# Kernel optimization log

Hardware: AMD Instinct MI355X
Metric: run time of the kernel (lower is better)

Reference implementation:

```python
import jax, jax.numpy as jnp
from jax import lax
import numpy as np

B, H, W, D_MODEL = 2, 64, 64, 192
D_INNER, D_STATE, DT_RANK = 384, 16, 12
L = H * W
LN_EPS = 1e-5


def setup_inputs() -> dict:
    ks = jax.random.split(jax.random.key(0), 12)
    rng = np.random.default_rng(0)
    perm = rng.permutation(L).astype(np.int32)

    def p(i, shape, scale=0.02):
        return jax.random.normal(ks[i], shape, dtype=jnp.float32) * scale

    return {
        "x": jax.random.normal(ks[0], (B, H, W, D_MODEL), dtype=jnp.float32),
        "condition": jax.random.normal(ks[1], (B, H, W, D_MODEL), dtype=jnp.float32),
        "W_in": p(2, (2 * D_INNER, D_MODEL)),
        "W_con": p(3, (D_INNER, D_MODEL)),
        "conv_w": p(4, (D_INNER, 1, 3, 3)),
        "conv_b": jnp.zeros((D_INNER,), jnp.float32),
        "con_conv_w": p(5, (D_INNER, 1, 3, 3)),
        "con_conv_b": jnp.zeros((D_INNER,), jnp.float32),
        "x_proj_w": p(6, (DT_RANK + 2 * D_STATE, D_INNER)),
        "dt_proj_w": p(7, (D_INNER, DT_RANK)),
        "dt_proj_b": p(8, (D_INNER,), 0.1),
        "A_logs": jnp.tile(jnp.log(jnp.arange(1, D_STATE + 1, dtype=jnp.float32))[None, :], (D_INNER, 1)),
        "Ds": jnp.ones((D_INNER,), jnp.float32),
        "ln_w": jnp.ones((D_INNER,), jnp.float32),
        "ln_b": jnp.zeros((D_INNER,), jnp.float32),
        "W_out": p(9, (D_MODEL, D_INNER)),
        "scan_path": jnp.asarray(perm),
        "rev_scan_path": jnp.asarray(np.argsort(perm).astype(np.int32)),
    }


def _dwconv(x, w, b):
    # depthwise 3x3 conv, SAME padding; x: [B, C, H, W], w: [C, 1, 3, 3]
    y = lax.conv_general_dilated(x, w, (1, 1), "SAME",
                                 dimension_numbers=("NCHW", "OIHW", "NCHW"),
                                 feature_group_count=x.shape[1])
    return y + b[None, :, None, None]


def _selective_scan(u, delta, A, Bs, Cs, D):
    # u, delta: [B, D, L]; A: [D, N]; Bs, Cs: [B, N, L]; D: [D]
    dA = jnp.exp(jnp.einsum("bdl,dn->lbdn", delta, A))          # [L, B, D, N]
    dBu = jnp.einsum("bdl,bnl,bdl->lbdn", delta, Bs, u)          # [L, B, D, N]
    Ct = jnp.transpose(Cs, (2, 0, 1))                             # [L, B, N]
    h0 = jnp.zeros(dA.shape[1:], dA.dtype)

    def step(h, inp):
        a, b, c = inp
        h = a * h + b
        return h, jnp.einsum("bdn,bn->bd", h, c)

    _, ys = lax.scan(step, h0, (dA, dBu, Ct))                     # ys: [L, B, D]
    y = jnp.transpose(ys, (1, 2, 0))                              # [B, D, L]
    return y + u * D[None, :, None]


def _forward(x, condition, W_in, W_con, conv_w, conv_b, con_conv_w, con_conv_b,
             x_proj_w, dt_proj_w, dt_proj_b, A_logs, Ds, ln_w, ln_b, W_out,
             scan_path, rev_scan_path):
    b, h, w, _ = x.shape
    l = h * w
    xz = x @ W_in.T                                               # [B, H, W, 2*Din]
    xa, z = jnp.split(xz, 2, axis=-1)
    z = jax.nn.silu(z)
    c = condition @ W_con.T
    xa = jax.nn.silu(_dwconv(jnp.transpose(xa, (0, 3, 1, 2)), conv_w, conv_b))
    c = jax.nn.silu(_dwconv(jnp.transpose(c, (0, 3, 1, 2)), con_conv_w, con_conv_b))
    d = xa.shape[1]
    xs = xa.reshape(b, d, l)[:, :, scan_path]                     # forward_permutation, K=1
    cs = c.reshape(b, d, l)[:, :, scan_path]
    x_dbl = jnp.einsum("bdl,cd->bcl", xs + cs, x_proj_w)          # [B, R+2N, L]
    r, n = dt_proj_w.shape[1], A_logs.shape[1]
    dts = jnp.einsum("brl,dr->bdl", x_dbl[:, :r], dt_proj_w)
    Bs = x_dbl[:, r:r + n]
    Cs = x_dbl[:, r + n:]
    A = -jnp.exp(A_logs)
    delta = jax.nn.softplus(dts + dt_proj_b[None, :, None])       # delta_softplus=True
    y = _selective_scan(xs, delta, A, Bs, Cs, Ds)                 # [B, D, L]
    y = y[:, :, rev_scan_path]                                    # backward_permutation
    y = jnp.transpose(y, (0, 2, 1))                               # [B, L, D]
    mu = jnp.mean(y, axis=-1, keepdims=True)
    var = jnp.var(y, axis=-1, keepdims=True)
    y = (y - mu) * lax.rsqrt(var + LN_EPS) * ln_w + ln_b          # out_norm
    y = y.reshape(b, h, w, d) * z
    return y @ W_out.T                                            # out_proj (no bias)


def reference(x, condition, W_in, W_con, conv_w, conv_b, con_conv_w, con_conv_b,
              x_proj_w, dt_proj_w, dt_proj_b, A_logs, Ds, ln_w, ln_b, W_out,
              scan_path, rev_scan_path):
    return _forward(x, condition, W_in, W_con, conv_w, conv_b, con_conv_w,
                    con_conv_b, x_proj_w, dt_proj_w, dt_proj_b, A_logs, Ds,
                    ln_w, ln_b, W_out, scan_path, rev_scan_path)
```

## Files before the change

kernel.cpp:

```cpp
#include <hip/hip_runtime.h>
#include <math.h>

#define BB 2
#define HH 64
#define WW 64
#define DM 192
#define DI 384
#define NS 16
#define DTR 12
#define LL 4096
#define ROWS (BB*LL)
#define NCHUNK 128
#define LCHUNK 32
#define NCOMB 448
#define CSTRIDE ((size_t)BB * DI * 8)

typedef __attribute__((ext_vector_type(8))) short bf16x8;
typedef __attribute__((ext_vector_type(4))) float f32x4;

typedef __attribute__((address_space(3))) void        as3_void;
typedef __attribute__((address_space(1))) const void  as1_cvoid;

__device__ __forceinline__ void gl_lds16(const unsigned short* g, unsigned short* l) {
    __builtin_amdgcn_global_load_lds((as1_cvoid*)g, (as3_void*)l, 16, 0, 0);
}

__device__ __forceinline__ float silu_f(float v) {
    return v / (1.0f + __expf(-v));
}

__device__ __forceinline__ unsigned short f2bf(float f) {
    union { float f; unsigned int u; } c; c.f = f;
    unsigned int u = c.u;
    u += 0x7fffu + ((u >> 16) & 1u);
    return (unsigned short)(u >> 16);
}
__device__ __forceinline__ float bf2f(unsigned short h) {
    union { unsigned int u; float f; } c; c.u = ((unsigned int)h) << 16;
    return c.f;
}

__global__ __launch_bounds__(256) void prep_weights(
    const float* __restrict__ x, const float* __restrict__ cond,
    const float* __restrict__ w_in, const float* __restrict__ w_con,
    const float* __restrict__ w_out,
    const float* __restrict__ x_proj_w, const float* __restrict__ dt_w,
    unsigned short* __restrict__ w_in_bf, unsigned short* __restrict__ w_con_bf,
    unsigned short* __restrict__ w_out_bf, unsigned short* __restrict__ wc,
    unsigned short* __restrict__ x_bfo, unsigned short* __restrict__ c_bfo)
{
    int idx = blockIdx.x * 256 + threadIdx.x;
    if (idx < 73728) {
        const float4* src; ushort4* dst; int off;
        if (idx < 36864)      { src = (const float4*)w_in;  dst = (ushort4*)w_in_bf;  off = idx; }
        else if (idx < 55296) { src = (const float4*)w_con; dst = (ushort4*)w_con_bf; off = idx - 36864; }
        else                  { src = (const float4*)w_out; dst = (ushort4*)w_out_bf; off = idx - 55296; }
        float4 v = src[off];
        ushort4 o;
        o.x = f2bf(v.x); o.y = f2bf(v.y); o.z = f2bf(v.z); o.w = f2bf(v.w);
        dst[off] = o;
    } else if (idx < 73728 + NCOMB * DI) {
        int e = idx - 73728;
        int row = e / DI, k = e - row * DI;
        float v = 0.f;
        if (row < 384) {
            const float* dw = dt_w + row * DTR;
            #pragma unroll
            for (int r = 0; r < DTR; ++r) v += dw[r] * x_proj_w[r * DI + k];
        } else if (row < 416) {
            v = x_proj_w[(12 + (row - 384)) * DI + k];
        }
        wc[e] = f2bf(v);
    } else if (idx < 73728 + NCOMB * DI + 786432) {
        int e = idx - (73728 + NCOMB * DI);
        const float4* src; ushort4* dst; int off;
        if (e < 393216) { src = (const float4*)x;    dst = (ushort4*)x_bfo; off = e; }
        else            { src = (const float4*)cond; dst = (ushort4*)c_bfo; off = e - 393216; }
        float4 v = src[off];
        ushort4 o;
        o.x = f2bf(v.x); o.y = f2bf(v.y); o.z = f2bf(v.z); o.w = f2bf(v.w);
        dst[off] = o;
    }
}

__global__ __launch_bounds__(256) void gemm_in(
    const unsigned short* __restrict__ x_bf, const unsigned short* __restrict__ cin_bf,
    const unsigned short* __restrict__ w_in_bf,
    const unsigned short* __restrict__ w_con_bf,
    unsigned short* __restrict__ xa_bf, unsigned short* __restrict__ z_bf,
    unsigned short* __restrict__ c_bf)
{
    const int zz = blockIdx.z;
    if (zz == 1 && blockIdx.y >= 6) return;
    const unsigned short* A = zz ? cin_bf : x_bf;
    const unsigned short* W = zz ? w_con_bf : w_in_bf;

    __shared__ __align__(16) unsigned short sA[128 * 32];
    __shared__ __align__(16) unsigned short sB[64 * 32];
    const int bm = blockIdx.x * 128;
    const int bn = blockIdx.y * 64;
    const int tid  = threadIdx.x;
    const int wave = tid >> 6;
    const int lane = tid & 63;
    const int quad = lane >> 4;
    const int l16  = lane & 15;
    const int srow = tid >> 2;
    const int scol = (tid & 3) * 8;

    f32x4 acc[2][4];
    #pragma unroll
    for (int rf = 0; rf < 2; ++rf)
        #pragma unroll
        for (int t = 0; t < 4; ++t) acc[rf][t] = (f32x4)(0.f);

    const unsigned short* gA0 = &A[(size_t)(bm + srow) * DM + scol];
    const unsigned short* gA1 = gA0 + (size_t)64 * DM;
    const unsigned short* gB  = &W[(size_t)(bn + srow) * DM + scol];
    unsigned short* lA0 = &sA[wave * 512];
    unsigned short* lA1 = &sA[2048 + wave * 512];
    unsigned short* lB  = &sB[wave * 512];

    const int ar0 = (wave * 32 + l16) * 32 + quad * 8;
    const int ar1 = ar0 + 16 * 32;

    for (int k0 = 0; k0 < DM; k0 += 32) {
        gl_lds16(gA0 + k0, lA0);
        gl_lds16(gA1 + k0, lA1);
        gl_lds16(gB  + k0, lB);
        __syncthreads();
        bf16x8 a0 = *(bf16x8*)&sA[ar0];
        bf16x8 a1 = *(bf16x8*)&sA[ar1];
        #pragma unroll
        for (int t = 0; t < 4; ++t) {
            bf16x8 b = *(bf16x8*)&sB[(t * 16 + l16) * 32 + quad * 8];
            acc[0][t] = __builtin_amdgcn_mfma_f32_16x16x32_bf16(a0, b, acc[0][t], 0, 0, 0);
            acc[1][t] = __builtin_amdgcn_mfma_f32_16x16x32_bf16(a1, b, acc[1][t], 0, 0, 0);
        }
        __syncthreads();
    }

    #pragma unroll
    for (int rf = 0; rf < 2; ++rf) {
        #pragma unroll
        for (int t = 0; t < 4; ++t) {
            int col = bn + t * 16 + l16;
            #pragma unroll
            for (int r = 0; r < 4; ++r) {
                int row = bm + wave * 32 + rf * 16 + quad * 4 + r;
                float v = acc[rf][t][r];
                if (zz == 0) {
                    if (col < 384) xa_bf[(size_t)row * 384 + col] = f2bf(v);
                    else           z_bf[(size_t)row * 384 + (col - 384)] = f2bf(silu_f(v));
                } else {
                    c_bf[(size_t)row * 384 + col] = f2bf(v);
                }
            }
        }
    }
}

__global__ __launch_bounds__(256) void gemm_comb(
    const unsigned short* __restrict__ A, const unsigned short* __restrict__ W,
    const float* __restrict__ bias, float* __restrict__ btct,
    unsigned short* __restrict__ du_lo)
{
    __shared__ __align__(16) unsigned short sA[128 * 32];
    __shared__ __align__(16) unsigned short sB[64 * 32];
    const int bm = blockIdx.x * 128;
    const int bn = blockIdx.y * 64;
    const int tid  = threadIdx.x;
    const int wave = tid >> 6;
    const int lane = tid & 63;
    const int quad = lane >> 4;
    const int l16  = lane & 15;
    const int srow = tid >> 2;
    const int scol = (tid & 3) * 8;

    f32x4 acc[2][4];
    #pragma unroll
    for (int rf = 0; rf < 2; ++rf)
        #pragma unroll
        for (int t = 0; t < 4; ++t) acc[rf][t] = (f32x4)(0.f);

    const unsigned short* gA0 = &A[(size_t)(bm + srow) * DI + scol];
    const unsigned short* gA1 = gA0 + (size_t)64 * DI;
    const unsigned short* gB  = &W[(size_t)(bn + srow) * DI + scol];
    unsigned short* lA0 = &sA[wave * 512];
    unsigned short* lA1 = &sA[2048 + wave * 512];
    unsigned short* lB  = &sB[wave * 512];

    const int ar0 = (wave * 32 + l16) * 32 + quad * 8;
    const int ar1 = ar0 + 16 * 32;

    for (int k0 = 0; k0 < DI; k0 += 32) {
        gl_lds16(gA0 + k0, lA0);
        gl_lds16(gA1 + k0, lA1);
        gl_lds16(gB  + k0, lB);
        __syncthreads();
        bf16x8 a0 = *(bf16x8*)&sA[ar0];
        bf16x8 a1 = *(bf16x8*)&sA[ar1];
        #pragma unroll
        for (int t = 0; t < 4; ++t) {
            bf16x8 b = *(bf16x8*)&sB[(t * 16 + l16) * 32 + quad * 8];
            acc[0][t] = __builtin_amdgcn_mfma_f32_16x16x32_bf16(a0, b, acc[0][t], 0, 0, 0);
            acc[1][t] = __builtin_amdgcn_mfma_f32_16x16x32_bf16(a1, b, acc[1][t], 0, 0, 0);
        }
        __syncthreads();
    }

    #pragma unroll
    for (int rf = 0; rf < 2; ++rf) {
        #pragma unroll
        for (int t = 0; t < 4; ++t) {
            int col = bn + t * 16 + l16;
            #pragma unroll
            for (int r = 0; r < 4; ++r) {
                int row = bm + wave * 32 + rf * 16 + quad * 4 + r;
                float v = acc[rf][t][r];
                if (col < 384) {
                    float a = v + bias[col];
                    float sp = (a > 20.f) ? a : log1pf(__expf(a));
                    du_lo[((size_t)row * 384 + col) * 2] = f2bf(sp);
                } else if (col < 416) {
                    int idx = col - 384;
                    int pos = (idx < 16) ? ((idx & 7) * 4 + (idx >> 3))
                                         : (((idx - 16) & 7) * 4 + 2 + ((idx - 16) >> 3));
                    btct[(size_t)row * 32 + pos] = v;
                }
            }
        }
    }
}

__global__ __launch_bounds__(256) void gemm_outk(
    const unsigned short* __restrict__ A, const unsigned short* __restrict__ W,
    float* __restrict__ out)
{
    __shared__ __align__(16) unsigned short sA[64 * 32];
    __shared__ __align__(16) unsigned short sB[64 * 32];
    const int bm = blockIdx.x * 64;
    const int bn = blockIdx.y * 64;
    const int tid  = threadIdx.x;
    const int wave = tid >> 6;
    const int lane = tid & 63;
    const int quad = lane >> 4;
    const int l16  = lane & 15;
    const int srow = tid >> 2;
    const int scol = (tid & 3) * 8;

    f32x4 acc[4];
    #pragma unroll
    for (int t = 0; t < 4; ++t) acc[t] = (f32x4)(0.f);

    const unsigned short* gA = &A[(size_t)(bm + srow) * DI + scol];
    const unsigned short* gB = &W[(size_t)(bn + srow) * DI + scol];
    unsigned short* lA = &sA[wave * 512];
    unsigned short* lB = &sB[wave * 512];

    const int arow = (wave * 16 + l16) * 32 + quad * 8;

    for (int k0 = 0; k0 < DI; k0 += 32) {
        gl_lds16(gA + k0, lA);
        gl_lds16(gB + k0, lB);
        __syncthreads();
        bf16x8 a = *(bf16x8*)&sA[arow];
        #pragma unroll
        for (int t = 0; t < 4; ++t) {
            bf16x8 b = *(bf16x8*)&sB[(t * 16 + l16) * 32 + quad * 8];
            acc[t] = __builtin_amdgcn_mfma_f32_16x16x32_bf16(a, b, acc[t], 0, 0, 0);
        }
        __syncthreads();
    }

    #pragma unroll
    for (int t = 0; t < 4; ++t) {
        int col = bn + t * 16 + l16;
        #pragma unroll
        for (int r = 0; r < 4; ++r) {
            int row = bm + wave * 16 + quad * 4 + r;
            out[(size_t)row * DM + col] = acc[t][r];
        }
    }
}

__global__ __launch_bounds__(256) void dwconv2_scatter(
    const unsigned short* __restrict__ xin, const unsigned short* __restrict__ cin,
    const float* __restrict__ wx, const float* __restrict__ bx,
    const float* __restrict__ wc, const float* __restrict__ bc,
    const int* __restrict__ rev_scan_path,
    unsigned short* __restrict__ du_hi,
    unsigned short* __restrict__ s_bf)
{
    const int tile = blockIdx.x;
    const int c0   = blockIdx.y * 32;
    const int b    = blockIdx.z;
    const int h0 = (tile >> 3) * 8, w0 = (tile & 7) * 8;
    __shared__ float smx[10 * 10 * 32];
    __shared__ float smc[10 * 10 * 32];
    __shared__ int   jtile[64];

    for (int idx = threadIdx.x; idx < 3200; idx += 256) {
        int pix = idx >> 5, ch = idx & 31;
        int py = pix / 10, px = pix - py * 10;
        int gh = h0 + py - 1, gw = w0 + px - 1;
        float vx = 0.f, vc = 0.f;
        if (gh >= 0 && gh < 64 && gw >= 0 && gw < 64) {
            size_t g = ((size_t)(b * LL + gh * 64 + gw)) * DI + c0 + ch;
            vx = bf2f(xin[g]); vc = bf2f(cin[g]);
        }
        smx[idx] = vx; smc[idx] = vc;
    }
    if (threadIdx.x < 64) {
        int l = (h0 + (threadIdx.x >> 3)) * 64 + (w0 + (threadIdx.x & 7));
        jtile[threadIdx.x] = rev_scan_path[l];
    }
    __syncthreads();

    const int ch = threadIdx.x & 31;
    const int pq = threadIdx.x >> 5;
    float wrx[9], wrc[9];
    #pragma unroll
    for (int k = 0; k < 9; ++k) {
        wrx[k] = wx[(c0 + ch) * 9 + k];
        wrc[k] = wc[(c0 + ch) * 9 + k];
    }
    const float bvx = bx[c0 + ch];
    const float bvc = bc[c0 + ch];

    #pragma unroll
    for (int i = 0; i < 8; ++i) {
        int p  = pq * 8 + i;
        int ph = p >> 3, pw = p & 7;
        float ax = bvx, ac = bvc;
        #pragma unroll
        for (int ki = 0; ki < 3; ++ki)
            #pragma unroll
            for (int kj = 0; kj < 3; ++kj) {
                int si = ((ph + ki) * 10 + (pw + kj)) * 32 + ch;
                ax += wrx[ki * 3 + kj] * smx[si];
                ac += wrc[ki * 3 + kj] * smc[si];
            }
        float xv = silu_f(ax);
        float sv = xv + silu_f(ac);
        size_t o = ((size_t)(b * LL + jtile[p])) * DI + c0 + ch;
        du_hi[o * 2 + 1] = f2bf(xv);
        s_bf[o]          = f2bf(sv);
    }
}

__global__ __launch_bounds__(256) void scan_chunkA(
    const unsigned int* __restrict__ du, const float* __restrict__ btct,
    const float* __restrict__ A_logs,
    float* __restrict__ chunkA, float* __restrict__ chunkB)
{
    const int c = blockIdx.x;
    const int g = blockIdx.y;
    const int b = blockIdx.z;
    const int t = threadIdx.x;
    const int grp = t >> 3, p = t & 7;
    const int d = g * 32 + grp;
    const float Av0 = -__expf(A_logs[d * NS + p]);
    const float Av1 = -__expf(A_logs[d * NS + p + 8]);
    const int j0 = c * LCHUNK;

    const unsigned int* dul = du + ((size_t)b * LL + j0) * DI + d;
    const float2*       bl  = (const float2*)btct + ((size_t)b * LL + j0) * 16 + p * 2;

    float h0 = 0.f, h1 = 0.f, Sd = 0.f;
    unsigned int duv[4]; float2 bv[4];
    #pragma unroll
    for (int q = 0; q < 4; ++q) {
        duv[q] = dul[(size_t)q * DI]; bv[q] = bl[(size_t)q * 16];
    }
    for (int j = 0; j < LCHUNK; j += 4) {
        unsigned int ndu[4]; float2 nb[4];
        if (j + 4 < LCHUNK) {
            #pragma unroll
            for (int q = 0; q < 4; ++q) {
                int jj = j + 4 + q;
                ndu[q] = dul[(size_t)jj * DI]; nb[q] = bl[(size_t)jj * 16];
            }
        }
        #pragma unroll
        for (int q = 0; q < 4; ++q) {
            float dv = bf2f((unsigned short)(duv[q] & 0xffff));
            float uv = bf2f((unsigned short)(duv[q] >> 16));
            float e0 = __expf(dv * Av0);
            float e1 = __expf(dv * Av1);
            float duu = dv * uv;
            h0 = e0 * h0 + bv[q].x * duu;
            h1 = e1 * h1 + bv[q].y * duu;
            Sd += dv;
        }
        #pragma unroll
        for (int q = 0; q < 4; ++q) { duv[q]=ndu[q]; bv[q]=nb[q]; }
    }
    size_t idx = (size_t)c * CSTRIDE + ((size_t)b * DI + d) * 8 + p;
    ((float2*)chunkA)[idx] = make_float2(__expf(Sd * Av0), __expf(Sd * Av1));
    ((float2*)chunkB)[idx] = make_float2(h0, h1);
}

__global__ __launch_bounds__(256) void scan_chunkC(
    const unsigned int* __restrict__ du, const float* __restrict__ btct,
    const float* __restrict__ A_logs, const float* __restrict__ Ds,
    const float* __restrict__ chunkA, const float* __restrict__ chunkB,
    unsigned short* __restrict__ yt)
{
    const int c = blockIdx.x;
    const int g = blockIdx.y;
    const int b = blockIdx.z;
    const int t = threadIdx.x;
    const int grp = t >> 3, p = t & 7;
    const int d = g * 32 + grp;
    const float Av0 = -__expf(A_logs[d * NS + p]);
    const float Av1 = -__expf(A_logs[d * NS + p + 8]);
    const float Dv = Ds[d];
    const int j0 = c * LCHUNK;

    const unsigned int* dul = du + ((size_t)b * LL + j0) * DI + d;
    const float4*       bcl = (const float4*)btct + ((size_t)b * LL + j0) * 8 + p;
    unsigned short* yl = yt + ((size_t)b * LL + j0) * DI + d;

    const size_t off = ((size_t)b * DI + d) * 8 + p;
    const float2* A2 = (const float2*)chunkA;
    const float2* B2 = (const float2*)chunkB;
    float h0 = 0.f, h1 = 0.f, P0 = 1.f, P1 = 1.f;
    for (int i = c - 1; i >= 0; --i) {
        size_t ix = (size_t)i * CSTRIDE + off;
        float2 a = A2[ix], bv = B2[ix];
        h0 += P0 * bv.x;  h1 += P1 * bv.y;
        P0 *= a.x;        P1 *= a.y;
        if (fmaxf(fabsf(P0), fabsf(P1)) < 1e-30f) break;
    }

    unsigned int duv[4]; float4 bc[4];
    #pragma unroll
    for (int q = 0; q < 4; ++q) {
        duv[q] = dul[(size_t)q * DI]; bc[q] = bcl[(size_t)q * 8];
    }
    for (int j = 0; j < LCHUNK; j += 4) {
        unsigned int ndu[4]; float4 nbc[4];
        if (j + 4 < LCHUNK) {
            #pragma unroll
            for (int q = 0; q < 4; ++q) {
                int jj = j + 4 + q;
                ndu[q] = dul[(size_t)jj * DI]; nbc[q] = bcl[(size_t)jj * 8];
            }
        }
        #pragma unroll
        for (int q = 0; q < 4; ++q) {
            float dv = bf2f((unsigned short)(duv[q] & 0xffff));
            float uv = bf2f((unsigned short)(duv[q] >> 16));
            float e0 = __expf(dv * Av0);
            float e1 = __expf(dv * Av1);
            float duu = dv * uv;
            h0 = e0 * h0 + bc[q].x * duu;
            h1 = e1 * h1 + bc[q].y * duu;
            float acc = h0 * bc[q].z + h1 * bc[q].w;
            acc += __shfl_xor(acc, 4, 8);
            acc += __shfl_xor(acc, 2, 8);
            acc += __shfl_xor(acc, 1, 8);
            if (p == 0) yl[(size_t)(j + q) * DI] = f2bf(acc + uv * Dv);
        }
        #pragma unroll
        for (int q = 0; q < 4; ++q) { duv[q]=ndu[q]; bc[q]=nbc[q]; }
    }
}

__global__ __launch_bounds__(128) void ln_mul(
    const unsigned short* __restrict__ yt, const unsigned short* __restrict__ z,
    const int* __restrict__ scan_path,
    const float* __restrict__ ln_w, const float* __restrict__ ln_b,
    unsigned short* __restrict__ yn)
{
    const int j = blockIdx.x;
    const int b = blockIdx.y;
    const int l = scan_path[j];
    const int t = threadIdx.x;
    const unsigned short* row = yt + ((size_t)(b * LL + j)) * DI;
    float v0 = bf2f(row[t]), v1 = bf2f(row[t + 128]), v2 = bf2f(row[t + 256]);
    float s  = v0 + v1 + v2;
    float s2 = v0*v0 + v1*v1 + v2*v2;
    #pragma unroll
    for (int off = 32; off > 0; off >>= 1) {
        s  += __shfl_down(s, off);
        s2 += __shfl_down(s2, off);
    }
    __shared__ float red[4];
    if ((t & 63) == 0) { red[(t >> 6) * 2] = s; red[(t >> 6) * 2 + 1] = s2; }
    __syncthreads();
    float S  = red[0] + red[2];
    float S2 = red[1] + red[3];
    float mu  = S * (1.0f / DI);
    float var = S2 * (1.0f / DI) - mu * mu;
    float inv = rsqrtf(var + 1e-5f);

    const unsigned short* zr = z + ((size_t)(b * LL + l)) * DI;
    unsigned short* o = yn + ((size_t)(b * LL + l)) * DI;
    o[t]       = f2bf(((v0 - mu) * inv * ln_w[t]       + ln_b[t])       * bf2f(zr[t]));
    o[t + 128] = f2bf(((v1 - mu) * inv * ln_w[t + 128] + ln_b[t + 128]) * bf2f(zr[t + 128]));
    o[t + 256] = f2bf(((v2 - mu) * inv * ln_w[t + 256] + ln_b[t + 256]) * bf2f(zr[t + 256]));
}

extern "C" void kernel_launch(void* const* d_in, const int* in_sizes, int n_in,
                              void* d_out, int out_size, void* d_ws, size_t ws_size,
                              hipStream_t stream) {
    const float* x          = (const float*)d_in[0];
    const float* cond       = (const float*)d_in[1];
    const float* W_in       = (const float*)d_in[2];
    const float* W_con      = (const float*)d_in[3];
    const float* conv_w     = (const float*)d_in[4];
    const float* conv_b     = (const float*)d_in[5];
    const float* con_conv_w = (const float*)d_in[6];
    const float* con_conv_b = (const float*)d_in[7];
    const float* x_proj_w   = (const float*)d_in[8];
    const float* dt_proj_w  = (const float*)d_in[9];
    const float* dt_proj_b  = (const float*)d_in[10];
    const float* A_logs     = (const float*)d_in[11];
    const float* Ds         = (const float*)d_in[12];
    const float* ln_w       = (const float*)d_in[13];
    const float* ln_b       = (const float*)d_in[14];
    const float* W_out      = (const float*)d_in[15];
    const int*   scan_path  = (const int*)d_in[16];
    const int*   rev_path   = (const int*)d_in[17];

    float* ws = (float*)d_ws;
    const size_t S  = (size_t)BB * LL * DI;
    const size_t SC = (size_t)NCHUNK * BB * DI * NS;
    float* ytslab  = ws + 0 * S;
    float* zslab   = ws + 1 * S;
    float* ynslab  = ws + 2 * S;
    float* duslab  = ws + 3 * S;
    float* btct    = ws + 4 * S;
    float* chunkA  = btct + (size_t)BB * LL * 32;
    float* chunkB  = chunkA + SC;
    float* bfpool  = chunkB + SC;

    unsigned short* yt_bf    = (unsigned short*)ytslab;
    unsigned short* z_bf     = (unsigned short*)zslab;
    unsigned short* yn_bf    = (unsigned short*)ynslab;
    unsigned int*   du       = (unsigned int*)duslab;
    unsigned short* s_bf     = (unsigned short*)bfpool;
    unsigned short* xa_bf    = s_bf + (size_t)ROWS * DI;
    unsigned short* c_bf     = xa_bf + (size_t)ROWS * DI;
    unsigned short* w_in_bf  = c_bf + (size_t)ROWS * DI;
    unsigned short* w_con_bf = w_in_bf + 768 * DM;
    unsigned short* w_out_bf = w_con_bf + 384 * DM;
    unsigned short* wcomb_bf = w_out_bf + 192 * DI;
    unsigned short* x_bf2    = wcomb_bf + (size_t)NCOMB * DI;
    unsigned short* cin_bf2  = x_bf2 + (size_t)ROWS * DM;

    prep_weights<<<4032, 256, 0, stream>>>(
        x, cond, W_in, W_con, W_out, x_proj_w, dt_proj_w,
        w_in_bf, w_con_bf, w_out_bf, wcomb_bf, x_bf2, cin_bf2);

    gemm_in<<<dim3(ROWS / 128, 12, 2), 256, 0, stream>>>(
        x_bf2, cin_bf2, w_in_bf, w_con_bf, xa_bf, z_bf, c_bf);
    dwconv2_scatter<<<dim3(64, 12, BB), 256, 0, stream>>>(
        xa_bf, c_bf, conv_w, conv_b, con_conv_w, con_conv_b,
        rev_path, (unsigned short*)du, s_bf);
    gemm_comb<<<dim3(ROWS / 128, NCOMB / 64), 256, 0, stream>>>(
        s_bf, wcomb_bf, dt_proj_b, btct, (unsigned short*)du);
    scan_chunkA<<<dim3(NCHUNK, DI / 32, BB), 256, 0, stream>>>(
        du, btct, A_logs, chunkA, chunkB);
    scan_chunkC<<<dim3(NCHUNK, DI / 32, BB), 256, 0, stream>>>(
        du, btct, A_logs, Ds, chunkA, chunkB, yt_bf);
    ln_mul<<<dim3(LL, BB), 128, 0, stream>>>(yt_bf, z_bf, scan_path, ln_w, ln_b, yn_bf);
    gemm_outk<<<dim3(ROWS / 64, DM / 64), 256, 0, stream>>>(yn_bf, w_out_bf, (float*)d_out);
}
```

Before: 206.6 us.

## Fuse LayerNorm and gating into out-projection GEMM, widen input GEMM tiles

```diff
diff --git a/kernel.cpp b/kernel.cpp
--- a/kernel.cpp
+++ b/kernel.cpp
@@ -12,7 +12,7 @@
 #define ROWS (BB*LL)
 #define NCHUNK 128
 #define LCHUNK 32
-#define NCOMB 448
+#define NCOMBP 512
 #define CSTRIDE ((size_t)BB * DI * 8)
 
 typedef __attribute__((ext_vector_type(8))) short bf16x8;
@@ -59,7 +59,7 @@
         ushort4 o;
         o.x = f2bf(v.x); o.y = f2bf(v.y); o.z = f2bf(v.z); o.w = f2bf(v.w);
         dst[off] = o;
-    } else if (idx < 73728 + NCOMB * DI) {
+    } else if (idx < 73728 + NCOMBP * DI) {
         int e = idx - 73728;
         int row = e / DI, k = e - row * DI;
         float v = 0.f;
@@ -71,8 +71,8 @@
             v = x_proj_w[(12 + (row - 384)) * DI + k];
         }
         wc[e] = f2bf(v);
-    } else if (idx < 73728 + NCOMB * DI + 786432) {
-        int e = idx - (73728 + NCOMB * DI);
+    } else if (idx < 73728 + NCOMBP * DI + 786432) {
+        int e = idx - (73728 + NCOMBP * DI);
         const float4* src; ushort4* dst; int off;
         if (e < 393216) { src = (const float4*)x;    dst = (ushort4*)x_bfo; off = e; }
         else            { src = (const float4*)cond; dst = (ushort4*)c_bfo; off = e - 393216; }
@@ -91,14 +91,14 @@
     unsigned short* __restrict__ c_bf)
 {
     const int zz = blockIdx.z;
-    if (zz == 1 && blockIdx.y >= 6) return;
+    if (zz == 1 && blockIdx.y >= 3) return;
     const unsigned short* A = zz ? cin_bf : x_bf;
     const unsigned short* W = zz ? w_con_bf : w_in_bf;
 
     __shared__ __align__(16) unsigned short sA[128 * 32];
-    __shared__ __align__(16) unsigned short sB[64 * 32];
+    __shared__ __align__(16) unsigned short sB[128 * 32];
     const int bm = blockIdx.x * 128;
-    const int bn = blockIdx.y * 64;
+    const int bn = blockIdx.y * 128;
     const int tid  = threadIdx.x;
     const int wave = tid >> 6;
     const int lane = tid & 63;
@@ -107,18 +107,20 @@
     const int srow = tid >> 2;
     const int scol = (tid & 3) * 8;
 
-    f32x4 acc[2][4];
+    f32x4 acc[2][8];
     #pragma unroll
     for (int rf = 0; rf < 2; ++rf)
         #pragma unroll
-        for (int t = 0; t < 4; ++t) acc[rf][t] = (f32x4)(0.f);
+        for (int t = 0; t < 8; ++t) acc[rf][t] = (f32x4)(0.f);
 
     const unsigned short* gA0 = &A[(size_t)(bm + srow) * DM + scol];
     const unsigned short* gA1 = gA0 + (size_t)64 * DM;
-    const unsigned short* gB  = &W[(size_t)(bn + srow) * DM + scol];
+    const unsigned short* gB0 = &W[(size_t)(bn + srow) * DM + scol];
+    const unsigned short* gB1 = gB0 + (size_t)64 * DM;
     unsigned short* lA0 = &sA[wave * 512];
     unsigned short* lA1 = &sA[2048 + wave * 512];
-    unsigned short* lB  = &sB[wave * 512];
+    unsigned short* lB0 = &sB[wave * 512];
+    unsigned short* lB1 = &sB[2048 + wave * 512];
 
     const int ar0 = (wave * 32 + l16) * 32 + quad * 8;
     const int ar1 = ar0 + 16 * 32;
@@ -126,12 +128,13 @@
     for (int k0 = 0; k0 < DM; k0 += 32) {
         gl_lds16(gA0 + k0, lA0);
         gl_lds16(gA1 + k0, lA1);
-        gl_lds16(gB  + k0, lB);
+        gl_lds16(gB0 + k0, lB0);
+        gl_lds16(gB1 + k0, lB1);
         __syncthreads();
         bf16x8 a0 = *(bf16x8*)&sA[ar0];
         bf16x8 a1 = *(bf16x8*)&sA[ar1];
         #pragma unroll
-        for (int t = 0; t < 4; ++t) {
+        for (int t = 0; t < 8; ++t) {
             bf16x8 b = *(bf16x8*)&sB[(t * 16 + l16) * 32 + quad * 8];
             acc[0][t] = __builtin_amdgcn_mfma_f32_16x16x32_bf16(a0, b, acc[0][t], 0, 0, 0);
             acc[1][t] = __builtin_amdgcn_mfma_f32_16x16x32_bf16(a1, b, acc[1][t], 0, 0, 0);
@@ -142,7 +145,7 @@
     #pragma unroll
     for (int rf = 0; rf < 2; ++rf) {
         #pragma unroll
-        for (int t = 0; t < 4; ++t) {
+        for (int t = 0; t < 8; ++t) {
             int col = bn + t * 16 + l16;
             #pragma unroll
             for (int r = 0; r < 4; ++r) {
@@ -165,9 +168,9 @@
     unsigned short* __restrict__ du_lo)
 {
     __shared__ __align__(16) unsigned short sA[128 * 32];
-    __shared__ __align__(16) unsigned short sB[64 * 32];
+    __shared__ __align__(16) unsigned short sB[128 * 32];
     const int bm = blockIdx.x * 128;
-    const int bn = blockIdx.y * 64;
+    const int bn = blockIdx.y * 128;
     const int tid  = threadIdx.x;
     const int wave = tid >> 6;
     const int lane = tid & 63;
@@ -176,18 +179,20 @@
     const int srow = tid >> 2;
     const int scol = (tid & 3) * 8;
 
-    f32x4 acc[2][4];
+    f32x4 acc[2][8];
     #pragma unroll
     for (int rf = 0; rf < 2; ++rf)
         #pragma unroll
-        for (int t = 0; t < 4; ++t) acc[rf][t] = (f32x4)(0.f);
+        for (int t = 0; t < 8; ++t) acc[rf][t] = (f32x4)(0.f);
 
     const unsigned short* gA0 = &A[(size_t)(bm + srow) * DI + scol];
     const unsigned short* gA1 = gA0 + (size_t)64 * DI;
-    const unsigned short* gB  = &W[(size_t)(bn + srow) * DI + scol];
+    const unsigned short* gB0 = &W[(size_t)(bn + srow) * DI + scol];
+    const unsigned short* gB1 = gB0 + (size_t)64 * DI;
     unsigned short* lA0 = &sA[wave * 512];
     unsigned short* lA1 = &sA[2048 + wave * 512];
-    unsigned short* lB  = &sB[wave * 512];
+    unsigned short* lB0 = &sB[wave * 512];
+    unsigned short* lB1 = &sB[2048 + wave * 512];
 
     const int ar0 = (wave * 32 + l16) * 32 + quad * 8;
     const int ar1 = ar0 + 16 * 32;
@@ -195,12 +200,13 @@
     for (int k0 = 0; k0 < DI; k0 += 32) {
         gl_lds16(gA0 + k0, lA0);
         gl_lds16(gA1 + k0, lA1);
-        gl_lds16(gB  + k0, lB);
+        gl_lds16(gB0 + k0, lB0);
+        gl_lds16(gB1 + k0, lB1);
         __syncthreads();
         bf16x8 a0 = *(bf16x8*)&sA[ar0];
         bf16x8 a1 = *(bf16x8*)&sA[ar1];
         #pragma unroll
-        for (int t = 0; t < 4; ++t) {
+        for (int t = 0; t < 8; ++t) {
             bf16x8 b = *(bf16x8*)&sB[(t * 16 + l16) * 32 + quad * 8];
             acc[0][t] = __builtin_amdgcn_mfma_f32_16x16x32_bf16(a0, b, acc[0][t], 0, 0, 0);
             acc[1][t] = __builtin_amdgcn_mfma_f32_16x16x32_bf16(a1, b, acc[1][t], 0, 0, 0);
@@ -211,7 +217,7 @@
     #pragma unroll
     for (int rf = 0; rf < 2; ++rf) {
         #pragma unroll
-        for (int t = 0; t < 4; ++t) {
+        for (int t = 0; t < 8; ++t) {
             int col = bn + t * 16 + l16;
             #pragma unroll
             for (int r = 0; r < 4; ++r) {
@@ -232,42 +238,83 @@
     }
 }
 
-__global__ __launch_bounds__(256) void gemm_outk(
-    const unsigned short* __restrict__ A, const unsigned short* __restrict__ W,
-    float* __restrict__ out)
-{
-    __shared__ __align__(16) unsigned short sA[64 * 32];
+__global__ __launch_bounds__(256) void gemm_out_fused(
+    const unsigned short* __restrict__ yt, const unsigned short* __restrict__ z,
+    const int* __restrict__ rev_path,
+    const float* __restrict__ ln_w, const float* __restrict__ ln_b,
+    const unsigned short* __restrict__ W, float* __restrict__ out)
+{
+    __shared__ __align__(16) unsigned short sA[64 * 392];
     __shared__ __align__(16) unsigned short sB[64 * 32];
     const int bm = blockIdx.x * 64;
     const int bn = blockIdx.y * 64;
-    const int tid  = threadIdx.x;
+    const int tid = threadIdx.x;
+    const int r   = tid >> 2;
+    const int q4  = tid & 3;
+    const int b   = bm >> 12;
+    const int l   = (bm & (LL - 1)) + r;
+    const int js  = rev_path[l];
+
+    const unsigned short* yrow = yt + ((size_t)(b * LL + js)) * DI;
+    const unsigned short* zrow = z  + ((size_t)(b * LL + l)) * DI;
+
+    float s = 0.f, s2 = 0.f;
+    #pragma unroll
+    for (int i = 0; i < 12; ++i) {
+        bf16x8 v = *(const bf16x8*)&yrow[i * 32 + q4 * 8];
+        #pragma unroll
+        for (int e = 0; e < 8; ++e) {
+            float f = bf2f((unsigned short)v[e]);
+            s += f; s2 += f * f;
+        }
+    }
+    s  += __shfl_xor(s, 1);  s  += __shfl_xor(s, 2);
+    s2 += __shfl_xor(s2, 1); s2 += __shfl_xor(s2, 2);
+    const float mu  = s * (1.0f / DI);
+    const float inv = rsqrtf(s2 * (1.0f / DI) - mu * mu + 1e-5f);
+
+    #pragma unroll
+    for (int i = 0; i < 12; ++i) {
+        int c = i * 32 + q4 * 8;
+        bf16x8 v  = *(const bf16x8*)&yrow[c];
+        bf16x8 zv = *(const bf16x8*)&zrow[c];
+        float4 wa = *(const float4*)&ln_w[c];
+        float4 wb = *(const float4*)&ln_w[c + 4];
+        float4 ba = *(const float4*)&ln_b[c];
+        float4 bb = *(const float4*)&ln_b[c + 4];
+        bf16x8 o;
+        o[0] = (short)f2bf(((bf2f((unsigned short)v[0]) - mu) * inv * wa.x + ba.x) * bf2f((unsigned short)zv[0]));
+        o[1] = (short)f2bf(((bf2f((unsigned short)v[1]) - mu) * inv * wa.y + ba.y) * bf2f((unsigned short)zv[1]));
+        o[2] = (short)f2bf(((bf2f((unsigned short)v[2]) - mu) * inv * wa.z + ba.z) * bf2f((unsigned short)zv[2]));
+        o[3] = (short)f2bf(((bf2f((unsigned short)v[3]) - mu) * inv * wa.w + ba.w) * bf2f((unsigned short)zv[3]));
+        o[4] = (short)f2bf(((bf2f((unsigned short)v[4]) - mu) * inv * wb.x + bb.x) * bf2f((unsigned short)zv[4]));
+        o[5] = (short)f2bf(((bf2f((unsigned short)v[5]) - mu) * inv * wb.y + bb.y) * bf2f((unsigned short)zv[5]));
+        o[6] = (short)f2bf(((bf2f((unsigned short)v[6]) - mu) * inv * wb.z + bb.z) * bf2f((unsigned short)zv[6]));
+        o[7] = (short)f2bf(((bf2f((unsigned short)v[7]) - mu) * inv * wb.w + bb.w) * bf2f((unsigned short)zv[7]));
+        *(bf16x8*)&sA[r * 392 + c] = o;
+    }
+
     const int wave = tid >> 6;
     const int lane = tid & 63;
     const int quad = lane >> 4;
     const int l16  = lane & 15;
-    const int srow = tid >> 2;
-    const int scol = (tid & 3) * 8;
 
     f32x4 acc[4];
     #pragma unroll
     for (int t = 0; t < 4; ++t) acc[t] = (f32x4)(0.f);
 
-    const unsigned short* gA = &A[(size_t)(bm + srow) * DI + scol];
-    const unsigned short* gB = &W[(size_t)(bn + srow) * DI + scol];
-    unsigned short* lA = &sA[wave * 512];
+    const unsigned short* gB = &W[(size_t)(bn + r) * DI + q4 * 8];
     unsigned short* lB = &sB[wave * 512];
-
-    const int arow = (wave * 16 + l16) * 32 + quad * 8;
+    const int abase = (wave * 16 + l16) * 392 + quad * 8;
 
     for (int k0 = 0; k0 < DI; k0 += 32) {
-        gl_lds16(gA + k0, lA);
         gl_lds16(gB + k0, lB);
         __syncthreads();
-        bf16x8 a = *(bf16x8*)&sA[arow];
+        bf16x8 a = *(bf16x8*)&sA[abase + k0];
         #pragma unroll
         for (int t = 0; t < 4; ++t) {
-            bf16x8 b = *(bf16x8*)&sB[(t * 16 + l16) * 32 + quad * 8];
-            acc[t] = __builtin_amdgcn_mfma_f32_16x16x32_bf16(a, b, acc[t], 0, 0, 0);
+            bf16x8 bfr = *(bf16x8*)&sB[(t * 16 + l16) * 32 + quad * 8];
+            acc[t] = __builtin_amdgcn_mfma_f32_16x16x32_bf16(a, bfr, acc[t], 0, 0, 0);
         }
         __syncthreads();
     }
@@ -276,9 +323,9 @@
     for (int t = 0; t < 4; ++t) {
         int col = bn + t * 16 + l16;
         #pragma unroll
-        for (int r = 0; r < 4; ++r) {
-            int row = bm + wave * 16 + quad * 4 + r;
-            out[(size_t)row * DM + col] = acc[t][r];
+        for (int rr = 0; rr < 4; ++rr) {
+            int row = bm + wave * 16 + quad * 4 + rr;
+            out[(size_t)row * DM + col] = acc[t][rr];
         }
     }
 }
@@ -465,41 +512,6 @@
         #pragma unroll
         for (int q = 0; q < 4; ++q) { duv[q]=ndu[q]; bc[q]=nbc[q]; }
     }
-}
-
-__global__ __launch_bounds__(128) void ln_mul(
-    const unsigned short* __restrict__ yt, const unsigned short* __restrict__ z,
-    const int* __restrict__ scan_path,
-    const float* __restrict__ ln_w, const float* __restrict__ ln_b,
-    unsigned short* __restrict__ yn)
-{
-    const int j = blockIdx.x;
-    const int b = blockIdx.y;
-    const int l = scan_path[j];
-    const int t = threadIdx.x;
-    const unsigned short* row = yt + ((size_t)(b * LL + j)) * DI;
-    float v0 = bf2f(row[t]), v1 = bf2f(row[t + 128]), v2 = bf2f(row[t + 256]);
-    float s  = v0 + v1 + v2;
-    float s2 = v0*v0 + v1*v1 + v2*v2;
-    #pragma unroll
-    for (int off = 32; off > 0; off >>= 1) {
-        s  += __shfl_down(s, off);
-        s2 += __shfl_down(s2, off);
-    }
-    __shared__ float red[4];
-    if ((t & 63) == 0) { red[(t >> 6) * 2] = s; red[(t >> 6) * 2 + 1] = s2; }
-    __syncthreads();
-    float S  = red[0] + red[2];
-    float S2 = red[1] + red[3];
-    float mu  = S * (1.0f / DI);
-    float var = S2 * (1.0f / DI) - mu * mu;
-    float inv = rsqrtf(var + 1e-5f);
-
-    const unsigned short* zr = z + ((size_t)(b * LL + l)) * DI;
-    unsigned short* o = yn + ((size_t)(b * LL + l)) * DI;
-    o[t]       = f2bf(((v0 - mu) * inv * ln_w[t]       + ln_b[t])       * bf2f(zr[t]));
-    o[t + 128] = f2bf(((v1 - mu) * inv * ln_w[t + 128] + ln_b[t + 128]) * bf2f(zr[t + 128]));
-    o[t + 256] = f2bf(((v2 - mu) * inv * ln_w[t + 256] + ln_b[t + 256]) * bf2f(zr[t + 256]));
 }
 
 extern "C" void kernel_launch(void* const* d_in, const int* in_sizes, int n_in,
@@ -523,22 +535,21 @@
     const float* W_out      = (const float*)d_in[15];
     const int*   scan_path  = (const int*)d_in[16];
     const int*   rev_path   = (const int*)d_in[17];
+    (void)scan_path;
 
     float* ws = (float*)d_ws;
     const size_t S  = (size_t)BB * LL * DI;
     const size_t SC = (size_t)NCHUNK * BB * DI * NS;
     float* ytslab  = ws + 0 * S;
     float* zslab   = ws + 1 * S;
-    float* ynslab  = ws + 2 * S;
-    float* duslab  = ws + 3 * S;
-    float* btct    = ws + 4 * S;
+    float* duslab  = ws + 2 * S;
+    float* btct    = ws + 3 * S;
     float* chunkA  = btct + (size_t)BB * LL * 32;
     float* chunkB  = chunkA + SC;
     float* bfpool  = chunkB + SC;
 
     unsigned short* yt_bf    = (unsigned short*)ytslab;
     unsigned short* z_bf     = (unsigned short*)zslab;
-    unsigned short* yn_bf    = (unsigned short*)ynslab;
     unsigned int*   du       = (unsigned int*)duslab;
     unsigned short* s_bf     = (unsigned short*)bfpool;
     unsigned short* xa_bf    = s_bf + (size_t)ROWS * DI;
@@ -547,24 +558,24 @@
     unsigned short* w_con_bf = w_in_bf + 768 * DM;
     unsigned short* w_out_bf = w_con_bf + 384 * DM;
     unsigned short* wcomb_bf = w_out_bf + 192 * DI;
-    unsigned short* x_bf2    = wcomb_bf + (size_t)NCOMB * DI;
+    unsigned short* x_bf2    = wcomb_bf + (size_t)NCOMBP * DI;
     unsigned short* cin_bf2  = x_bf2 + (size_t)ROWS * DM;
 
-    prep_weights<<<4032, 256, 0, stream>>>(
+    prep_weights<<<4128, 256, 0, stream>>>(
         x, cond, W_in, W_con, W_out, x_proj_w, dt_proj_w,
         w_in_bf, w_con_bf, w_out_bf, wcomb_bf, x_bf2, cin_bf2);
 
-    gemm_in<<<dim3(ROWS / 128, 12, 2), 256, 0, stream>>>(
+    gemm_in<<<dim3(ROWS / 128, 6, 2), 256, 0, stream>>>(
         x_bf2, cin_bf2, w_in_bf, w_con_bf, xa_bf, z_bf, c_bf);
     dwconv2_scatter<<<dim3(64, 12, BB), 256, 0, stream>>>(
         xa_bf, c_bf, conv_w, conv_b, con_conv_w, con_conv_b,
         rev_path, (unsigned short*)du, s_bf);
-    gemm_comb<<<dim3(ROWS / 128, NCOMB / 64), 256, 0, stream>>>(
+    gemm_comb<<<dim3(ROWS / 128, NCOMBP / 128), 256, 0, stream>>>(
         s_bf, wcomb_bf, dt_proj_b, btct, (unsigned short*)du);
     scan_chunkA<<<dim3(NCHUNK, DI / 32, BB), 256, 0, stream>>>(
         du, btct, A_logs, chunkA, chunkB);
     scan_chunkC<<<dim3(NCHUNK, DI / 32, BB), 256, 0, stream>>>(
         du, btct, A_logs, Ds, chunkA, chunkB, yt_bf);
-    ln_mul<<<dim3(LL, BB), 128, 0, stream>>>(yt_bf, z_bf, scan_path, ln_w, ln_b, yn_bf);
-    gemm_outk<<<dim3(ROWS / 64, DM / 64), 256, 0, stream>>>(yn_bf, w_out_bf, (float*)d_out);
-}
+    gemm_out_fused<<<dim3(ROWS / 64, DM / 64), 256, 0, stream>>>(
+        yt_bf, z_bf, rev_path, ln_w, ln_b, w_out_bf, (float*)d_out);
+}
```

Result: slower. 227.4 us (+10.1%).
